# Kernel tuning notes

Hardware: AMD Instinct MI355X
Metric: run time of the kernel (lower is better)

The kernel has to match this reference:

```python
import jax, jax.numpy as jnp
import numpy as np

EMBED_DIM = 1024
NUM_HEADS = 16
HEAD_DIM = EMBED_DIM // NUM_HEADS
B, S = 2, 2048


def setup_inputs() -> dict:
    key = jax.random.key(0)
    ks = jax.random.split(key, 11)
    glorot = lambda k, shape: jax.random.normal(k, shape, jnp.float32) * (2.0 / sum(shape)) ** 0.5
    return {
        "query": jax.random.normal(ks[0], (B, S, EMBED_DIM), jnp.float32),
        "key": jax.random.normal(ks[1], (B, S, EMBED_DIM), jnp.float32),
        "value": jax.random.normal(ks[2], (B, S, EMBED_DIM), jnp.float32),
        "Wq": glorot(ks[3], (EMBED_DIM, EMBED_DIM)), "bq": jnp.zeros((EMBED_DIM,), jnp.float32),
        "Wk": glorot(ks[4], (EMBED_DIM, EMBED_DIM)), "bk": jnp.zeros((EMBED_DIM,), jnp.float32),
        "Wv": glorot(ks[5], (EMBED_DIM, EMBED_DIM)), "bv": jnp.zeros((EMBED_DIM,), jnp.float32),
        "Wo": glorot(ks[6], (EMBED_DIM, EMBED_DIM)), "bo": jnp.zeros((EMBED_DIM,), jnp.float32),
    }


def reference(query, key, value, Wq, bq, Wk, bk, Wv, bv, Wo, bo):
    b, s, _ = query.shape
    # QKV projections
    q = query @ Wq + bq
    k = key @ Wk + bk
    v = value @ Wv + bv
    # [B, S, H, D] -> [B, H, S, D]
    q = q.reshape(b, s, NUM_HEADS, HEAD_DIM).transpose(0, 2, 1, 3)
    k = k.reshape(b, s, NUM_HEADS, HEAD_DIM).transpose(0, 2, 1, 3)
    v = v.reshape(b, s, NUM_HEADS, HEAD_DIM).transpose(0, 2, 1, 3)
    # scores [B, H, S, S], materialized as in the original
    scores = jnp.einsum("bhqd,bhkd->bhqk", q, k) / jnp.sqrt(jnp.float32(HEAD_DIM))
    attn = jax.nn.softmax(scores, axis=-1)
    out = jnp.einsum("bhqk,bhkd->bhqd", attn, v)  # [B, H, S, D]
    out = out.transpose(0, 2, 1, 3).reshape(b, s, EMBED_DIM)
    return out @ Wo + bo
```

## Files before the change

kernel.cpp:

```cpp
#include <hip/hip_runtime.h>
#include <hip/hip_bf16.h>


#define EMBED 1024
#define NHEAD 16
#define HDIM 64
#define SEQ 2048
#define MROWS 4096

typedef __attribute__((ext_vector_type(8))) __bf16 bf16x8;
typedef __attribute__((ext_vector_type(4))) float f32x4;
typedef __attribute__((ext_vector_type(16))) float f32x16;

__device__ __forceinline__ unsigned short f2bf(float f) {
  unsigned int u = __builtin_bit_cast(unsigned int, f);
  u += 0x7fffu + ((u >> 16) & 1u);
  return (unsigned short)(u >> 16);
}

__device__ __forceinline__ int cvtpk_bf16(float lo, float hi) {
  int r;
  asm("v_cvt_pk_bf16_f32 %0, %1, %2" : "=v"(r) : "v"(lo), "v"(hi));
  return r;
}

__device__ __forceinline__ float max3f(float a, float b, float c) {
  return fmaxf(fmaxf(a, b), c);
}

__device__ __forceinline__ int swz(int row, int bcol) {
  return row * 128 + (bcol ^ ((row & 7) << 4));
}

__device__ __forceinline__ void gload16(const void* g, void* l) {
  __builtin_amdgcn_global_load_lds((const __attribute__((address_space(1))) void*)g,
                                   (__attribute__((address_space(3))) void*)l, 16, 0, 0);
}

__global__ __launch_bounds__(256) void cvt_f32_bf16(const float* __restrict__ i0, const float* __restrict__ i1,
                                                    const float* __restrict__ i2,
                                                    unsigned short* __restrict__ o0, unsigned short* __restrict__ o1,
                                                    unsigned short* __restrict__ o2) {
  const float* in; unsigned short* out;
  switch (blockIdx.y) {
    case 0: in = i0; out = o0; break;
    case 1: in = i1; out = o1; break;
    default: in = i2; out = o2; break;
  }
  int i = blockIdx.x * 256 + threadIdx.x;
  const float4* p = reinterpret_cast<const float4*>(in) + (size_t)i * 2;
  float4 a = p[0], b = p[1];
  int4 r;
  r.x = cvtpk_bf16(a.x, a.y);
  r.y = cvtpk_bf16(a.z, a.w);
  r.z = cvtpk_bf16(b.x, b.y);
  r.w = cvtpk_bf16(b.z, b.w);
  reinterpret_cast<int4*>(out)[i] = r;
}

__global__ __launch_bounds__(256) void wtrans(const float* __restrict__ w0, const float* __restrict__ w1,
                                              const float* __restrict__ w2, const float* __restrict__ w3,
                                              unsigned short* __restrict__ o0, unsigned short* __restrict__ o1,
                                              unsigned short* __restrict__ o2, unsigned short* __restrict__ o3) {
  __shared__ float tile[64][65];
  const float* src; unsigned short* dst;
  switch (blockIdx.z) {
    case 0: src = w0; dst = o0; break;
    case 1: src = w1; dst = o1; break;
    case 2: src = w2; dst = o2; break;
    default: src = w3; dst = o3; break;
  }
  const int k0 = blockIdx.y * 64, n0 = blockIdx.x * 64;
  const int c = threadIdx.x & 63, r0 = threadIdx.x >> 6;
#pragma unroll
  for (int i = 0; i < 16; ++i) {
    int r = r0 + i * 4;
    tile[r][c] = src[(size_t)(k0 + r) * EMBED + n0 + c];
  }
  __syncthreads();
#pragma unroll
  for (int i = 0; i < 16; ++i) {
    int nr = r0 + i * 4;
    dst[(size_t)(n0 + nr) * EMBED + k0 + c] = f2bf(tile[c][nr]);
  }
}

template <int BN>
__device__ __forceinline__ void gemm_core(const unsigned short* __restrict__ A,
                                          const unsigned short* __restrict__ Bt,
                                          const float* __restrict__ bias,
                                          void* __restrict__ C, float oscale, int mode) {
  constexpr int K = EMBED;
  constexpr int MF = (BN == 128) ? 4 : 2;
  constexpr int BRW = BN / 4;
  __shared__ __align__(16) unsigned short Alds[128 * 64];
  __shared__ __align__(16) unsigned short Blds[BN * 64];
  char* Ab8 = (char*)Alds; char* Bb8 = (char*)Blds;
  const char* AB = (const char*)A;
  const char* BB = (const char*)Bt;
  const int tid = threadIdx.x;
  const int lane = tid & 63, w = tid >> 6;
  const int wr = (BN == 128) ? (w >> 1) : w;
  const int wc = (BN == 128) ? (w & 1) : 0;
  const int fr = lane & 15, fq = lane >> 4;
  const int m0 = blockIdx.y * 128, n0 = blockIdx.x * BN;
  const int bcol = (lane & 7) * 16;
  const int gsc = bcol ^ ((lane >> 3) << 4);

  f32x4 acc[MF][4];
#pragma unroll
  for (int m = 0; m < MF; ++m)
#pragma unroll
    for (int n = 0; n < 4; ++n) acc[m][n] = f32x4{0.f, 0.f, 0.f, 0.f};

#define GSTAGE(k0_)                                                                          \
  {                                                                                          \
    _Pragma("unroll") for (int i_ = 0; i_ < 4; ++i_) {                                       \
      int row_ = w * 32 + i_ * 8 + (lane >> 3);                                              \
      gload16(AB + (size_t)(m0 + row_) * (K * 2) + (k0_)*2 + gsc, Ab8 + w * 4096 + i_ * 1024); \
    }                                                                                        \
    _Pragma("unroll") for (int i_ = 0; i_ < BRW / 8; ++i_) {                                 \
      int row_ = w * BRW + i_ * 8 + (lane >> 3);                                             \
      gload16(BB + (size_t)(n0 + row_) * (K * 2) + (k0_)*2 + gsc,                            \
              Bb8 + w * (BRW * 128) + i_ * 1024);                                            \
    }                                                                                        \
  }

  GSTAGE(0);

  for (int k0 = 0; k0 < K; k0 += 64) {
    __syncthreads();
    bf16x8 af2[2][MF], bf2[2][4];
#pragma unroll
    for (int ks = 0; ks < 2; ++ks) {
#pragma unroll
      for (int m = 0; m < MF; ++m) {
        int ar = wr * (MF * 16) + m * 16 + fr;
        af2[ks][m] = *reinterpret_cast<const bf16x8*>(Ab8 + swz(ar, ks * 64 + fq * 16));
      }
#pragma unroll
      for (int n = 0; n < 4; ++n) {
        int br = wc * 64 + n * 16 + fr;
        bf2[ks][n] = *reinterpret_cast<const bf16x8*>(Bb8 + swz(br, ks * 64 + fq * 16));
      }
    }
    __syncthreads();
    if (k0 + 64 < K) GSTAGE(k0 + 64);
#pragma unroll
    for (int ks = 0; ks < 2; ++ks)
#pragma unroll
      for (int m = 0; m < MF; ++m)
#pragma unroll
        for (int n = 0; n < 4; ++n)
          acc[m][n] = __builtin_amdgcn_mfma_f32_16x16x32_bf16(af2[ks][m], bf2[ks][n], acc[m][n], 0, 0, 0);
  }
#undef GSTAGE

#pragma unroll
  for (int n = 0; n < 4; ++n) {
    int col = n0 + wc * 64 + n * 16 + fr;
    float bv = bias[col];
#pragma unroll
    for (int m = 0; m < MF; ++m) {
      int rowb = m0 + wr * (MF * 16) + m * 16 + fq * 4;
      if (mode == 2) {
        int b = rowb >> 11, s0 = rowb & (SEQ - 1);
        int s0p = (s0 & ~12) | ((s0 & 4) << 1) | ((s0 & 8) >> 1);
        int h = col >> 6, d = col & 63;
        int2 pk;
        pk.x = cvtpk_bf16((acc[m][n][0] + bv) * oscale, (acc[m][n][1] + bv) * oscale);
        pk.y = cvtpk_bf16((acc[m][n][2] + bv) * oscale, (acc[m][n][3] + bv) * oscale);
        *reinterpret_cast<int2*>(
            &reinterpret_cast<unsigned short*>(C)[((size_t)((b * NHEAD + h) * HDIM + d)) * SEQ + s0p]) = pk;
      } else if (mode == 0) {
#pragma unroll
        for (int r = 0; r < 4; ++r) {
          int row = rowb + r;
          float v = (acc[m][n][r] + bv) * oscale;
          int b = row >> 11, s = row & (SEQ - 1), h = col >> 6, d = col & 63;
          reinterpret_cast<unsigned short*>(C)[((size_t)((b * NHEAD + h) * SEQ + s) << 6) + d] = f2bf(v);
        }
      } else {
#pragma unroll
        for (int r = 0; r < 4; ++r)
          reinterpret_cast<float*>(C)[(size_t)(rowb + r) * EMBED + col] = acc[m][n][r] + bv;
      }
    }
  }
}

__global__ __launch_bounds__(256) void gemm_qkv(
    const unsigned short* __restrict__ Xq, const unsigned short* __restrict__ Xk,
    const unsigned short* __restrict__ Xv,
    const unsigned short* __restrict__ Wqt, const unsigned short* __restrict__ Wkt,
    const unsigned short* __restrict__ Wvt,
    const float* __restrict__ bq, const float* __restrict__ bk, const float* __restrict__ bv,
    unsigned short* __restrict__ Qb, unsigned short* __restrict__ Kb,
    unsigned short* __restrict__ Vtb, float qscale) {
  switch (blockIdx.z) {
    case 0: gemm_core<128>(Xq, Wqt, bq, Qb, qscale, 0); break;
    case 1: gemm_core<128>(Xk, Wkt, bk, Kb, 1.0f, 0); break;
    default: gemm_core<128>(Xv, Wvt, bv, Vtb, 1.0f, 2); break;
  }
}

__global__ __launch_bounds__(256) void gemm_out(const unsigned short* __restrict__ A,
                                                const unsigned short* __restrict__ Bt,
                                                const float* __restrict__ bias,
                                                float* __restrict__ C) {
  gemm_core<64>(A, Bt, bias, C, 1.0f, 1);
}

__global__ __launch_bounds__(128) void attn(const unsigned short* __restrict__ Q,
                                            const unsigned short* __restrict__ Kk,
                                            const unsigned short* __restrict__ Vt,
                                            unsigned short* __restrict__ AO) {
  __shared__ __align__(16) unsigned short Klds[2][64 * 64];
  __shared__ __align__(16) unsigned short Vlds[2][64 * 64];
  const int tid = threadIdx.x, lane = tid & 63, w = tid >> 6;
  const int ql = lane & 31, t = lane >> 5;

  const int lin = blockIdx.x;
  const int head = (lin & 7) * 4 + ((lin >> 3) & 3);
  const int q0 = (lin >> 5) * 64;
  const size_t hb = (size_t)head * SEQ * HDIM;
  const unsigned short* Qh = Q + hb;
  const char* KhB = (const char*)(Kk + hb);
  const char* VhB = (const char*)(Vt + hb);

  const int gsc = ((lane & 7) * 16) ^ ((lane >> 3) << 4);
  const int row0 = w * 32 + (lane >> 3);

#define STAGE(kt_, b_)                                                                     \
  {                                                                                        \
    char* kb_ = (char*)Klds[b_];                                                           \
    char* vb_ = (char*)Vlds[b_];                                                           \
    _Pragma("unroll") for (int i_ = 0; i_ < 4; ++i_) {                                     \
      gload16(KhB + (size_t)((kt_)*64 + row0 + i_ * 8) * 128 + gsc,                        \
              kb_ + w * 4096 + i_ * 1024);                                                 \
      gload16(VhB + (size_t)(row0 + i_ * 8) * (SEQ * 2) + (kt_)*128 + gsc,                 \
              vb_ + w * 4096 + i_ * 1024);                                                 \
    }                                                                                      \
  }

  bf16x8 qf[4];
  {
    const unsigned short* qp = Qh + (size_t)(q0 + w * 32 + ql) * HDIM + t * 8;
    qf[0] = *reinterpret_cast<const bf16x8*>(qp);
    qf[1] = *reinterpret_cast<const bf16x8*>(qp + 16);
    qf[2] = *reinterpret_cast<const bf16x8*>(qp + 32);
    qf[3] = *reinterpret_cast<const bf16x8*>(qp + 48);
  }
  f32x16 oacc0 = {}, oacc1 = {};
  float mrow = -1e30f, lrow = 0.f;

  STAGE(0, 0);
  __syncthreads();

  for (int kt = 0; kt < SEQ / 64; ++kt) {
    const int cur = kt & 1;
    const bool more = (kt + 1 < SEQ / 64);
    if (more) STAGE(kt + 1, cur ^ 1);
    char* Kb8 = (char*)Klds[cur];
    char* Vb8 = (char*)Vlds[cur];

    f32x16 sc0 = {}, sc1 = {};
    __builtin_amdgcn_s_setprio(1);
#pragma unroll
    for (int s = 0; s < 4; ++s) {
      bf16x8 kf0 = *reinterpret_cast<const bf16x8*>(Kb8 + swz(ql, s * 32 + t * 16));
      bf16x8 kf1 = *reinterpret_cast<const bf16x8*>(Kb8 + swz(32 + ql, s * 32 + t * 16));
      sc0 = __builtin_amdgcn_mfma_f32_32x32x16_bf16(kf0, qf[s], sc0, 0, 0, 0);
      sc1 = __builtin_amdgcn_mfma_f32_32x32x16_bf16(kf1, qf[s], sc1, 0, 0, 0);
    }
    __builtin_amdgcn_s_setprio(0);

    float l1[12];
#pragma unroll
    for (int i = 0; i < 5; ++i) l1[i] = max3f(sc0[3 * i], sc0[3 * i + 1], sc0[3 * i + 2]);
#pragma unroll
    for (int i = 0; i < 5; ++i) l1[5 + i] = max3f(sc1[3 * i], sc1[3 * i + 1], sc1[3 * i + 2]);
    l1[10] = sc0[15];
    l1[11] = sc1[15];
    float l2a = max3f(l1[0], l1[1], l1[2]);
    float l2b = max3f(l1[3], l1[4], l1[5]);
    float l2c = max3f(l1[6], l1[7], l1[8]);
    float l2d = max3f(l1[9], l1[10], l1[11]);
    float mt = fmaxf(max3f(l2a, l2b, l2c), l2d);
    mt = fmaxf(mt, __shfl_xor(mt, 32));

    if (!__all(mt <= mrow + 8.0f)) {
      float mn = fmaxf(mrow, mt);
      float resc = __builtin_amdgcn_exp2f(mrow - mn);
      lrow *= resc;
#pragma unroll
      for (int r = 0; r < 16; ++r) {
        float rq = __shfl(resc, (r & 3) + 8 * (r >> 2) + 4 * t, 64);
        oacc0[r] *= rq;
        oacc1[r] *= rq;
      }
      mrow = mn;
    }

    float ps0 = 0.f, ps1 = 0.f, ps2 = 0.f, ps3 = 0.f;
#pragma unroll
    for (int i = 0; i < 4; ++i) {
      sc0[4 * i + 0] = __builtin_amdgcn_exp2f(sc0[4 * i + 0] - mrow);
      sc0[4 * i + 1] = __builtin_amdgcn_exp2f(sc0[4 * i + 1] - mrow);
      sc0[4 * i + 2] = __builtin_amdgcn_exp2f(sc0[4 * i + 2] - mrow);
      sc0[4 * i + 3] = __builtin_amdgcn_exp2f(sc0[4 * i + 3] - mrow);
      sc1[4 * i + 0] = __builtin_amdgcn_exp2f(sc1[4 * i + 0] - mrow);
      sc1[4 * i + 1] = __builtin_amdgcn_exp2f(sc1[4 * i + 1] - mrow);
      sc1[4 * i + 2] = __builtin_amdgcn_exp2f(sc1[4 * i + 2] - mrow);
      sc1[4 * i + 3] = __builtin_amdgcn_exp2f(sc1[4 * i + 3] - mrow);
      ps0 += sc0[4 * i + 0] + sc0[4 * i + 1];
      ps1 += sc0[4 * i + 2] + sc0[4 * i + 3];
      ps2 += sc1[4 * i + 0] + sc1[4 * i + 1];
      ps3 += sc1[4 * i + 2] + sc1[4 * i + 3];
    }
    lrow += (ps0 + ps1) + (ps2 + ps3);

    int4 paw[4];
#pragma unroll
    for (int s2 = 0; s2 < 2; ++s2) {
      paw[s2].x     = cvtpk_bf16(sc0[8 * s2 + 0], sc0[8 * s2 + 1]);
      paw[s2].y     = cvtpk_bf16(sc0[8 * s2 + 2], sc0[8 * s2 + 3]);
      paw[s2].z     = cvtpk_bf16(sc0[8 * s2 + 4], sc0[8 * s2 + 5]);
      paw[s2].w     = cvtpk_bf16(sc0[8 * s2 + 6], sc0[8 * s2 + 7]);
      paw[2 + s2].x = cvtpk_bf16(sc1[8 * s2 + 0], sc1[8 * s2 + 1]);
      paw[2 + s2].y = cvtpk_bf16(sc1[8 * s2 + 2], sc1[8 * s2 + 3]);
      paw[2 + s2].z = cvtpk_bf16(sc1[8 * s2 + 4], sc1[8 * s2 + 5]);
      paw[2 + s2].w = cvtpk_bf16(sc1[8 * s2 + 6], sc1[8 * s2 + 7]);
    }

    __builtin_amdgcn_s_setprio(1);
#pragma unroll
    for (int s = 0; s < 4; ++s) {
      bf16x8 pa = __builtin_bit_cast(bf16x8, paw[s]);
      bf16x8 v0 = *reinterpret_cast<const bf16x8*>(Vb8 + swz(ql, s * 32 + t * 16));
      bf16x8 v1 = *reinterpret_cast<const bf16x8*>(Vb8 + swz(32 + ql, s * 32 + t * 16));
      oacc0 = __builtin_amdgcn_mfma_f32_32x32x16_bf16(pa, v0, oacc0, 0, 0, 0);
      oacc1 = __builtin_amdgcn_mfma_f32_32x32x16_bf16(pa, v1, oacc1, 0, 0, 0);
    }
    __builtin_amdgcn_s_setprio(0);

    __syncthreads();
  }
#undef STAGE

  lrow += __shfl_xor(lrow, 32);

  const int b = head >> 4, hh = head & 15;
#pragma unroll
  for (int r = 0; r < 16; ++r) {
    int qr = (r & 3) + 8 * (r >> 2) + 4 * t;
    float inv = 1.0f / __shfl(lrow, qr, 64);
    int srow = q0 + w * 32 + qr;
    size_t ob = (size_t)(b * SEQ + srow) * EMBED + hh * 64 + ql;
    AO[ob] = f2bf(oacc0[r] * inv);
    AO[ob + 32] = f2bf(oacc1[r] * inv);
  }
}

extern "C" void kernel_launch(void* const* d_in, const int* in_sizes, int n_in,
                              void* d_out, int out_size, void* d_ws, size_t ws_size,
                              hipStream_t stream) {
  const float* q32 = (const float*)d_in[0];
  const float* k32 = (const float*)d_in[1];
  const float* v32 = (const float*)d_in[2];
  const float* Wq = (const float*)d_in[3]; const float* bq = (const float*)d_in[4];
  const float* Wk = (const float*)d_in[5]; const float* bk = (const float*)d_in[6];
  const float* Wv = (const float*)d_in[7]; const float* bv = (const float*)d_in[8];
  const float* Wo = (const float*)d_in[9]; const float* bo = (const float*)d_in[10];
  float* out = (float*)d_out;

  char* ws = (char*)d_ws;
  const size_t MB = 1u << 20;
  unsigned short* Xq  = (unsigned short*)(ws + 0 * MB);
  unsigned short* Xk  = (unsigned short*)(ws + 8 * MB);
  unsigned short* Xv  = (unsigned short*)(ws + 16 * MB);
  unsigned short* Wqt = (unsigned short*)(ws + 24 * MB);
  unsigned short* Wkt = (unsigned short*)(ws + 26 * MB);
  unsigned short* Wvt = (unsigned short*)(ws + 28 * MB);
  unsigned short* Wot = (unsigned short*)(ws + 30 * MB);
  unsigned short* Qb  = (unsigned short*)(ws + 32 * MB);
  unsigned short* Kb  = (unsigned short*)(ws + 40 * MB);
  unsigned short* Vtb = (unsigned short*)(ws + 48 * MB);
  unsigned short* AO  = Xq;

  const int n8 = (MROWS * EMBED) / 8;
  cvt_f32_bf16<<<dim3(n8 / 256, 3), 256, 0, stream>>>(q32, k32, v32, Xq, Xk, Xv);
  wtrans<<<dim3(16, 16, 4), 256, 0, stream>>>(Wq, Wk, Wv, Wo, Wqt, Wkt, Wvt, Wot);

  const float qscale = 0.125f * 1.44269504088896340736f;
  gemm_qkv<<<dim3(EMBED / 128, MROWS / 128, 3), 256, 0, stream>>>(
      Xq, Xk, Xv, Wqt, Wkt, Wvt, bq, bk, bv, Qb, Kb, Vtb, qscale);

  attn<<<dim3(SEQ / 64 * 32), 128, 0, stream>>>(Qb, Kb, Vtb, AO);

  gemm_out<<<dim3(EMBED / 64, MROWS / 128), 256, 0, stream>>>(AO, Wot, bo, out);
}
```

Before: 133.5 us.

## Merge conversion kernels and remap GEMM block IDs for XCD-aware L2 locality

Fuses the activation conversion and weight transpose kernels into one prep launch, which saves a kernel launch and the gap between the two. Both GEMM kernels now use a 1D grid with a remap (id&7)*N + id>>3. Because blocks are dispatched round-robin across the 8 XCDs, this places contiguous logical tiles on the same XCD so they share its L2 for A and B tiles. The cost is extra index arithmetic and a slightly more branchy prep kernel.

```diff
diff --git a/kernel.cpp b/kernel.cpp
--- a/kernel.cpp
+++ b/kernel.cpp
@@ -37,51 +37,54 @@
                                    (__attribute__((address_space(3))) void*)l, 16, 0, 0);
 }
 
-__global__ __launch_bounds__(256) void cvt_f32_bf16(const float* __restrict__ i0, const float* __restrict__ i1,
-                                                    const float* __restrict__ i2,
-                                                    unsigned short* __restrict__ o0, unsigned short* __restrict__ o1,
-                                                    unsigned short* __restrict__ o2) {
-  const float* in; unsigned short* out;
-  switch (blockIdx.y) {
-    case 0: in = i0; out = o0; break;
-    case 1: in = i1; out = o1; break;
-    default: in = i2; out = o2; break;
-  }
-  int i = blockIdx.x * 256 + threadIdx.x;
-  const float4* p = reinterpret_cast<const float4*>(in) + (size_t)i * 2;
-  float4 a = p[0], b = p[1];
-  int4 r;
-  r.x = cvtpk_bf16(a.x, a.y);
-  r.y = cvtpk_bf16(a.z, a.w);
-  r.z = cvtpk_bf16(b.x, b.y);
-  r.w = cvtpk_bf16(b.z, b.w);
-  reinterpret_cast<int4*>(out)[i] = r;
-}
-
-__global__ __launch_bounds__(256) void wtrans(const float* __restrict__ w0, const float* __restrict__ w1,
-                                              const float* __restrict__ w2, const float* __restrict__ w3,
-                                              unsigned short* __restrict__ o0, unsigned short* __restrict__ o1,
-                                              unsigned short* __restrict__ o2, unsigned short* __restrict__ o3) {
+__global__ __launch_bounds__(256) void prep(const float* __restrict__ q32, const float* __restrict__ k32,
+                                            const float* __restrict__ v32,
+                                            unsigned short* __restrict__ Xq, unsigned short* __restrict__ Xk,
+                                            unsigned short* __restrict__ Xv,
+                                            const float* __restrict__ w0, const float* __restrict__ w1,
+                                            const float* __restrict__ w2, const float* __restrict__ w3,
+                                            unsigned short* __restrict__ o0, unsigned short* __restrict__ o1,
+                                            unsigned short* __restrict__ o2, unsigned short* __restrict__ o3) {
   __shared__ float tile[64][65];
-  const float* src; unsigned short* dst;
-  switch (blockIdx.z) {
-    case 0: src = w0; dst = o0; break;
-    case 1: src = w1; dst = o1; break;
-    case 2: src = w2; dst = o2; break;
-    default: src = w3; dst = o3; break;
-  }
-  const int k0 = blockIdx.y * 64, n0 = blockIdx.x * 64;
-  const int c = threadIdx.x & 63, r0 = threadIdx.x >> 6;
-#pragma unroll
-  for (int i = 0; i < 16; ++i) {
-    int r = r0 + i * 4;
-    tile[r][c] = src[(size_t)(k0 + r) * EMBED + n0 + c];
-  }
-  __syncthreads();
-#pragma unroll
-  for (int i = 0; i < 16; ++i) {
-    int nr = r0 + i * 4;
-    dst[(size_t)(n0 + nr) * EMBED + k0 + c] = f2bf(tile[c][nr]);
+  const int id = blockIdx.x;
+  if (id < 6144) {
+    const float* in; unsigned short* out;
+    switch (id >> 11) {
+      case 0: in = q32; out = Xq; break;
+      case 1: in = k32; out = Xk; break;
+      default: in = v32; out = Xv; break;
+    }
+    int i = (id & 2047) * 256 + threadIdx.x;
+    const float4* p = reinterpret_cast<const float4*>(in) + (size_t)i * 2;
+    float4 a = p[0], b = p[1];
+    int4 r;
+    r.x = cvtpk_bf16(a.x, a.y);
+    r.y = cvtpk_bf16(a.z, a.w);
+    r.z = cvtpk_bf16(b.x, b.y);
+    r.w = cvtpk_bf16(b.z, b.w);
+    reinterpret_cast<int4*>(out)[i] = r;
+  } else {
+    const int wid = id - 6144;
+    const float* src; unsigned short* dst;
+    switch (wid >> 8) {
+      case 0: src = w0; dst = o0; break;
+      case 1: src = w1; dst = o1; break;
+      case 2: src = w2; dst = o2; break;
+      default: src = w3; dst = o3; break;
+    }
+    const int k0 = ((wid >> 4) & 15) * 64, n0 = (wid & 15) * 64;
+    const int c = threadIdx.x & 63, r0 = threadIdx.x >> 6;
+#pragma unroll
+    for (int i = 0; i < 16; ++i) {
+      int r = r0 + i * 4;
+      tile[r][c] = src[(size_t)(k0 + r) * EMBED + n0 + c];
+    }
+    __syncthreads();
+#pragma unroll
+    for (int i = 0; i < 16; ++i) {
+      int nr = r0 + i * 4;
+      dst[(size_t)(n0 + nr) * EMBED + k0 + c] = f2bf(tile[c][nr]);
+    }
   }
 }
 
@@ -89,7 +92,8 @@
 __device__ __forceinline__ void gemm_core(const unsigned short* __restrict__ A,
                                           const unsigned short* __restrict__ Bt,
                                           const float* __restrict__ bias,
-                                          void* __restrict__ C, float oscale, int mode) {
+                                          void* __restrict__ C, float oscale, int mode,
+                                          int m0, int n0) {
   constexpr int K = EMBED;
   constexpr int MF = (BN == 128) ? 4 : 2;
   constexpr int BRW = BN / 4;
@@ -103,7 +107,6 @@
   const int wr = (BN == 128) ? (w >> 1) : w;
   const int wc = (BN == 128) ? (w & 1) : 0;
   const int fr = lane & 15, fq = lane >> 4;
-  const int m0 = blockIdx.y * 128, n0 = blockIdx.x * BN;
   const int bcol = (lane & 7) * 16;
   const int gsc = bcol ^ ((lane >> 3) << 4);
 
@@ -197,10 +200,14 @@
     const float* __restrict__ bq, const float* __restrict__ bk, const float* __restrict__ bv,
     unsigned short* __restrict__ Qb, unsigned short* __restrict__ Kb,
     unsigned short* __restrict__ Vtb, float qscale) {
-  switch (blockIdx.z) {
-    case 0: gemm_core<128>(Xq, Wqt, bq, Qb, qscale, 0); break;
-    case 1: gemm_core<128>(Xk, Wkt, bk, Kb, 1.0f, 0); break;
-    default: gemm_core<128>(Xv, Wvt, bv, Vtb, 1.0f, 2); break;
+  const int id = blockIdx.x;
+  const int lg = (id & 7) * 96 + (id >> 3);
+  const int z = lg >> 8, rem = lg & 255;
+  const int m0 = (rem >> 3) * 128, n0 = (rem & 7) * 128;
+  switch (z) {
+    case 0: gemm_core<128>(Xq, Wqt, bq, Qb, qscale, 0, m0, n0); break;
+    case 1: gemm_core<128>(Xk, Wkt, bk, Kb, 1.0f, 0, m0, n0); break;
+    default: gemm_core<128>(Xv, Wvt, bv, Vtb, 1.0f, 2, m0, n0); break;
   }
 }
 
@@ -208,7 +215,10 @@
                                                 const unsigned short* __restrict__ Bt,
                                                 const float* __restrict__ bias,
                                                 float* __restrict__ C) {
-  gemm_core<64>(A, Bt, bias, C, 1.0f, 1);
+  const int id = blockIdx.x;
+  const int lg = (id & 7) * 64 + (id >> 3);
+  const int m0 = (lg >> 4) * 128, n0 = (lg & 15) * 64;
+  gemm_core<64>(A, Bt, bias, C, 1.0f, 1, m0, n0);
 }
 
 __global__ __launch_bounds__(128) void attn(const unsigned short* __restrict__ Q,
@@ -388,15 +398,14 @@
   unsigned short* Vtb = (unsigned short*)(ws + 48 * MB);
   unsigned short* AO  = Xq;
 
-  const int n8 = (MROWS * EMBED) / 8;
-  cvt_f32_bf16<<<dim3(n8 / 256, 3), 256, 0, stream>>>(q32, k32, v32, Xq, Xk, Xv);
-  wtrans<<<dim3(16, 16, 4), 256, 0, stream>>>(Wq, Wk, Wv, Wo, Wqt, Wkt, Wvt, Wot);
+  prep<<<7168, 256, 0, stream>>>(q32, k32, v32, Xq, Xk, Xv,
+                                 Wq, Wk, Wv, Wo, Wqt, Wkt, Wvt, Wot);
 
   const float qscale = 0.125f * 1.44269504088896340736f;
-  gemm_qkv<<<dim3(EMBED / 128, MROWS / 128, 3), 256, 0, stream>>>(
-      Xq, Xk, Xv, Wqt, Wkt, Wvt, bq, bk, bv, Qb, Kb, Vtb, qscale);
+  gemm_qkv<<<768, 256, 0, stream>>>(Xq, Xk, Xv, Wqt, Wkt, Wvt, bq, bk, bv,
+                                    Qb, Kb, Vtb, qscale);
 
   attn<<<dim3(SEQ / 64 * 32), 128, 0, stream>>>(Qb, Kb, Vtb, AO);
 
-  gemm_out<<<dim3(EMBED / 64, MROWS / 128), 256, 0, stream>>>(AO, Wot, bo, out);
-}
+  gemm_out<<<512, 256, 0, stream>>>(AO, Wot, bo, out);
+}
```

New measurement: 124.1 us, median of 2. 1.08x faster.
